# Kernel optimization log

Hardware: AMD Instinct MI355X
Metric: run time of the kernel (lower is better)

Reference implementation:

```python
import jax, jax.numpy as jnp
import numpy as np

N, E, B = 50000, 200000, 512
F0, H1, C2, EMB = 78, 10, 128, 128
SEQ, VOCAB, NF, KW = 1000, 26, 32, 8
LOUT = EMB - KW + 1  # 121


def setup_inputs() -> dict:
    key = jax.random.key(0)
    ks = jax.random.split(key, 20)
    nrm = lambda k, s: jax.random.normal(k, s, jnp.float32) * 0.05
    return dict(
        x=jax.random.normal(ks[0], (N, F0), jnp.float32),
        edge_index=jax.random.randint(ks[1], (2, E), 0, N),
        batch=(jnp.arange(N) * B) // N,  # balanced sorted node->graph ids, all segments non-empty
        target=jax.random.randint(ks[2], (B, SEQ), 0, VOCAB),
        W1=nrm(ks[3], (F0, H1 * F0)), a_src1=nrm(ks[4], (H1, F0)), a_dst1=nrm(ks[5], (H1, F0)), b1=jnp.zeros((H1 * F0,), jnp.float32),
        W2=nrm(ks[6], (H1 * F0, C2)), a_src2=nrm(ks[7], (1, C2)), a_dst2=nrm(ks[8], (1, C2)), b2=jnp.zeros((C2,), jnp.float32),
        fc_g1_w=nrm(ks[9], (C2, C2)), fc_g1_b=jnp.zeros((C2,), jnp.float32),
        emb=nrm(ks[10], (VOCAB, EMB)),
        conv_w=nrm(ks[11], (NF, SEQ, KW)), conv_b=jnp.zeros((NF,), jnp.float32),
        fc_xt_w=nrm(ks[12], (NF * LOUT, C2)), fc_xt_b=jnp.zeros((C2,), jnp.float32),
        fc1_w=nrm(ks[13], (2 * C2, 1024)), fc1_b=jnp.zeros((1024,), jnp.float32),
        fc2_w=nrm(ks[14], (1024, 256)), fc2_b=jnp.zeros((256,), jnp.float32),
        out_w=nrm(ks[15], (256, 1)), out_b=jnp.zeros((1,), jnp.float32),
    )


def gat_conv(x, src, dst, W, a_src, a_dst, b, heads):
    # PyG GATConv (eval mode): project, per-edge attn logits, segment softmax over dst, scatter-add
    n = x.shape[0]
    c = W.shape[1] // heads
    h = (x @ W).reshape(n, heads, c)                 # [N,H,C]
    al_s = (h * a_src).sum(-1)                       # [N,H]
    al_d = (h * a_dst).sum(-1)
    al = jax.nn.leaky_relu(al_s[src] + al_d[dst], 0.2)   # [E',H]
    amax = jax.ops.segment_max(al, dst, num_segments=n)
    ex = jnp.exp(al - amax[dst])
    den = jax.ops.segment_sum(ex, dst, num_segments=n)
    alpha = ex / (den[dst] + 1e-16)
    out = jax.ops.segment_sum(h[src] * alpha[:, :, None], dst, num_segments=n)  # [N,H,C]
    return out.reshape(n, heads * c) + b


def reference(x, edge_index, batch, target, W1, a_src1, a_dst1, b1, W2, a_src2, a_dst2, b2,
              fc_g1_w, fc_g1_b, emb, conv_w, conv_b, fc_xt_w, fc_xt_b,
              fc1_w, fc1_b, fc2_w, fc2_b, out_w, out_b):
    n = x.shape[0]
    loops = jnp.arange(n)
    src = jnp.concatenate([edge_index[0], loops])    # add self loops (PyG default)
    dst = jnp.concatenate([edge_index[1], loops])
    h = jax.nn.elu(gat_conv(x, src, dst, W1, a_src1, a_dst1, b1, H1))
    h = jax.nn.relu(gat_conv(h, src, dst, W2, a_src2, a_dst2, b2, 1))
    g = jax.ops.segment_max(h, batch, num_segments=B)            # global max pool per graph
    g = jax.nn.relu(g @ fc_g1_w + fc_g1_b)                       # [B,128]
    e = emb[target]                                              # [B,1000,128]
    conv = jax.lax.conv_general_dilated(e, conv_w, (1,), 'VALID',
                                        dimension_numbers=('NCH', 'OIH', 'NCH'))
    conv = jax.nn.relu(conv + conv_b[None, :, None])             # [B,32,121]
    xt = conv.reshape(B, NF * LOUT) @ fc_xt_w + fc_xt_b          # [B,128]
    xc = jnp.concatenate([g, xt], axis=1)                        # [B,256]
    xc = jax.nn.relu(xc @ fc1_w + fc1_b)
    xc = jax.nn.relu(xc @ fc2_w + fc2_b)
    return xc @ out_w + out_b                                    # [B,1]
```

## Files before the change

kernel.cpp:

```cpp
#include <hip/hip_runtime.h>
#include <hip/hip_bf16.h>

#define N_NODES 50000
#define N_EDGES 200000
#define BGRAPHS 512
#define F0c 78
#define H1c 10
#define HC1 780
#define HSTR 832
#define C2c 128
#define SEQc 1000
#define VOCABc 26
#define NFc 32
#define KWc 8
#define LOUTc 121
#define EMBc 128
#define KX 96
#define KXT 3872
#define KSTEPS2 13
#define MROWS 13312
#define KM 1024

typedef __attribute__((ext_vector_type(8))) short short8;
typedef __attribute__((ext_vector_type(4))) float f32x4;
typedef unsigned short u16;

static constexpr size_t alignup(size_t x) { return (x + 255) & ~size_t(255); }

static constexpr size_t A_HBUF = 0;
static constexpr size_t A_OUT1 = alignup(A_HBUF + size_t(N_NODES)*HSTR*2);
static constexpr size_t A_H2   = alignup(A_OUT1 + size_t(N_NODES)*HSTR*2);
static constexpr size_t A_W2T  = alignup(A_H2   + size_t(N_NODES)*C2c*4);
static constexpr size_t A_ALS1 = alignup(A_W2T  + size_t(C2c)*HSTR*2);
static constexpr size_t A_ALD1 = alignup(A_ALS1 + size_t(N_NODES)*H1c*4);
static constexpr size_t A_ALS2 = alignup(A_ALD1 + size_t(N_NODES)*H1c*4);
static constexpr size_t A_ALD2 = alignup(A_ALS2 + size_t(N_NODES)*4);
static constexpr size_t A_DEG  = alignup(A_ALD2 + size_t(N_NODES)*4);
static constexpr size_t A_OFFS = alignup(A_DEG  + size_t(N_NODES)*4);
static constexpr size_t A_CUR  = alignup(A_OFFS + size_t(N_NODES+1)*4);
static constexpr size_t A_CSRC = alignup(A_CUR  + size_t(N_NODES)*4);
static constexpr size_t A_XC   = alignup(A_CSRC + size_t(N_EDGES+N_NODES)*4);
static constexpr size_t A_Y1   = alignup(A_XC   + size_t(BGRAPHS)*256*4);
static constexpr size_t A_BOFF = alignup(A_Y1   + size_t(BGRAPHS)*1024*4);
static constexpr size_t A_BPAD = alignup(A_BOFF + size_t(BGRAPHS)*(VOCABc+1)*4);
static constexpr size_t A_WXT  = alignup(A_BPAD + size_t(HSTR)*4);
static constexpr size_t A_FXP  = alignup(A_WXT  + size_t(C2c)*KXT*2);
static constexpr size_t A_W1HP = alignup(A_FXP  + size_t(11)*BGRAPHS*C2c*4);
static constexpr size_t A_WSD  = alignup(A_W1HP + size_t(10)*80*96*2);
static constexpr size_t A_CWT  = alignup(A_WSD  + size_t(2)*H1c*F0c*4);
static constexpr size_t A_END  = alignup(A_CWT  + size_t(2)*256*KM*2);

static constexpr size_t A_HFIN = A_HBUF;
static constexpr size_t A_AMAT = alignup(A_HFIN + size_t(N_NODES)*C2c*4);
static constexpr size_t A_CVO  = alignup(A_AMAT + size_t(MROWS)*256*4);
static constexpr size_t A_M    = alignup(A_CVO  + size_t(BGRAPHS)*KXT*2);
static_assert(A_M + size_t(MROWS)*KM*2 <= size_t(N_NODES)*HSTR*2, "alias A overflow");
static constexpr size_t A_XPAD = A_OUT1;
static_assert(size_t(N_NODES)*KX*2 <= size_t(N_NODES)*HSTR*2, "alias B overflow");

__device__ __forceinline__ float bflo(unsigned u) { return __uint_as_float(u << 16); }
__device__ __forceinline__ float bfhi(unsigned u) { return __uint_as_float(u & 0xffff0000u); }
__device__ __forceinline__ u16 f2bf(float v) {
    __hip_bfloat16 b = __float2bfloat16(v);
    return *(u16*)&b;
}

#define GLOAD16(g, l) __builtin_amdgcn_global_load_lds( \
    (const __attribute__((address_space(1))) void*)(g), \
    (__attribute__((address_space(3))) void*)(l), 16, 0, 0)

__global__ void k_prep(const float* __restrict__ x, const float* __restrict__ W1,
                       const float* __restrict__ W2, const float* __restrict__ b1,
                       const float* __restrict__ fcxt_w, const float* __restrict__ conv_w,
                       const float* __restrict__ a_src1, const float* __restrict__ a_dst1,
                       __hip_bfloat16* __restrict__ xpad, __hip_bfloat16* __restrict__ w1hp,
                       __hip_bfloat16* __restrict__ w2t, float* __restrict__ bpad,
                       __hip_bfloat16* __restrict__ wxt, float* __restrict__ wsd,
                       u16* __restrict__ cwt, int* __restrict__ deg) {
    int i = blockIdx.x*256 + threadIdx.x;
    const int R0 = N_NODES;
    const int R1 = R0 + N_NODES*KX;
    const int R2 = R1 + 10*80*96;
    const int R3 = R2 + C2c*HSTR;
    const int R4 = R3 + HSTR;
    const int R5 = R4 + C2c*KXT;
    const int R6 = R5 + 2*H1c*F0c;
    const int R7 = R6 + 256*KM;
    if (i < R0) {
        deg[i] = 1;
    } else if (i < R1) {
        int t = i - R0; int n = t / KX, c = t - n*KX;
        xpad[t] = __float2bfloat16(c < F0c ? x[(size_t)n*F0c + c] : 0.f);
    } else if (i < R2) {
        int t = i - R1; int hh = t / 7680, rem = t - hh*7680;
        int j = rem / 96, k = rem - j*96;
        w1hp[t] = __float2bfloat16((j < F0c && k < F0c) ? W1[(size_t)k*HC1 + hh*F0c + j] : 0.f);
    } else if (i < R3) {
        int t = i - R2; int c = t / HSTR, p = t - c*HSTR;
        int hh = p / 80, cc = p - hh*80;
        w2t[t] = __float2bfloat16((hh < H1c && cc < F0c) ? W2[(size_t)(hh*F0c + cc)*C2c + c] : 0.f);
    } else if (i < R4) {
        int p = i - R3; int hh = p / 80, cc = p - hh*80;
        bpad[p] = (hh < H1c && cc < F0c) ? b1[hh*F0c + cc] : 0.f;
    } else if (i < R5) {
        int t = i - R4; int c = t / KXT, j = t - c*KXT;
        wxt[t] = __float2bfloat16(fcxt_w[(size_t)j*C2c + c]);
    } else if (i < R6) {
        int t = i - R5; int sd = t / (H1c*F0c), rem = t - sd*(H1c*F0c);
        int hh = rem / F0c, c = rem - hh*F0c;
        const float* a = sd ? a_dst1 : a_src1;
        float v = 0.f;
        for (int j = 0; j < F0c; j++) v += W1[(size_t)c*HC1 + hh*F0c + j] * a[hh*F0c + j];
        wsd[t] = v;
    } else if (i < R7) {
        int t = i - R6; int col = t >> 10, ii = t & (KM-1);
        int o = col >> 3, k = col & 7;
        float v = (ii < SEQc) ? conv_w[((size_t)o*SEQc + ii)*KWc + k] : 0.f;
        u16 h = f2bf(v);
        float hv = __uint_as_float((unsigned)h << 16);
        cwt[(size_t)col*KM + ii] = h;
        cwt[(size_t)256*KM + (size_t)col*KM + ii] = f2bf(v - hv);
    }
}
#define PREP_TOTAL (N_NODES + N_NODES*KX + 10*80*96 + C2c*HSTR + HSTR + C2c*KXT + 2*H1c*F0c + 256*KM)

__global__ void k_count(const int* __restrict__ ei, int* deg) {
    int i = blockIdx.x*256 + threadIdx.x;
    if (i < N_EDGES) atomicAdd(&deg[ei[N_EDGES + i]], 1);
}
__global__ void k_scan(const int* __restrict__ deg, int* __restrict__ off,
                       int* __restrict__ cur, int n) {
    __shared__ int wsum[16];
    __shared__ int s_carry;
    int tid = threadIdx.x, lane = tid & 63, wid = tid >> 6;
    if (tid == 0) s_carry = 0;
    __syncthreads();
    for (int base = 0; base < n; base += 1024) {
        int i = base + tid;
        int v0 = (i < n) ? deg[i] : 0;
        int v = v0;
        for (int d = 1; d < 64; d <<= 1) { int t = __shfl_up(v, d, 64); if (lane >= d) v += t; }
        if (lane == 63) wsum[wid] = v;
        __syncthreads();
        if (wid == 0) {
            int w = (lane < 16) ? wsum[lane] : 0;
            for (int d = 1; d < 16; d <<= 1) { int t = __shfl_up(w, d, 64); if (lane >= d) w += t; }
            if (lane < 16) wsum[lane] = w;
        }
        __syncthreads();
        int wprev = (wid > 0) ? wsum[wid-1] : 0;
        int carry = s_carry;
        if (i < n) { int o = carry + wprev + (v - v0); off[i] = o; cur[i] = o; }
        __syncthreads();
        if (tid == 0) s_carry = carry + wsum[15];
        __syncthreads();
    }
    if (tid == 0) off[n] = s_carry;
}
__global__ void k_fill(const int* __restrict__ ei, int* cur, int* __restrict__ csrc) {
    int i = blockIdx.x*256 + threadIdx.x;
    if (i < N_EDGES) {
        int s = ei[i], d = ei[N_EDGES + i];
        int p = atomicAdd(&cur[d], 1);
        csrc[p] = s;
    } else if (i < N_EDGES + N_NODES) {
        int n = i - N_EDGES;
        int p = atomicAdd(&cur[n], 1);
        csrc[p] = n;
    }
}
__global__ void k_sortcsr(const int* __restrict__ offs, int* __restrict__ csrc) {
    int n = blockIdx.x*256 + threadIdx.x;
    if (n >= N_NODES) return;
    int s = offs[n], e = offs[n+1];
    for (int i = s + 1; i < e; i++) {
        int v = csrc[i];
        int j = i - 1;
        while (j >= s && csrc[j] > v) { csrc[j+1] = csrc[j]; j--; }
        csrc[j+1] = v;
    }
}

__global__ void k_att1x(const float* __restrict__ x, const float* __restrict__ wsd,
                        float* __restrict__ als, float* __restrict__ ald) {
    int i = blockIdx.x*256 + threadIdx.x;
    if (i >= N_NODES*H1c) return;
    int n = i / H1c, hh = i - n*H1c;
    const float* xr = x + (size_t)n*F0c;
    const float* ws = wsd + hh*F0c;
    const float* wd = wsd + H1c*F0c + hh*F0c;
    float s1 = 0.f, s2 = 0.f;
    for (int c = 0; c < F0c; c++) { float v = xr[c]; s1 += v*ws[c]; s2 += v*wd[c]; }
    als[i] = s1; ald[i] = s2;
}

__global__ void k_agg1x(const unsigned* __restrict__ xpu, const float* __restrict__ als,
                        const float* __restrict__ ald, const int* __restrict__ offs,
                        const int* __restrict__ csrc, unsigned* __restrict__ xaggu) {
    constexpr int H = H1c;
    int dn = blockIdx.x, lane = threadIdx.x;
    int s = offs[dn], e = offs[dn+1], deg = e - s;
    __shared__ float wexp[64*H];
    __shared__ int   ssrc[64];
    __shared__ float ms[H], dinv_s[H];

    if (deg <= 64) {
        if (lane < deg) ssrc[lane] = csrc[s + lane];
        __syncthreads();
        for (int idx = lane; idx < deg*H; idx += 64) {
            int j = idx / H, hh = idx - j*H;
            float al = als[(size_t)ssrc[j]*H + hh] + ald[(size_t)dn*H + hh];
            wexp[idx] = (al >= 0.f) ? al : 0.2f*al;
        }
        __syncthreads();
        if (lane < H) {
            float m = -1e30f;
            for (int j = 0; j < deg; j++) m = fmaxf(m, wexp[j*H + lane]);
            float den = 0.f;
            for (int j = 0; j < deg; j++) den += __expf(wexp[j*H + lane] - m);
            ms[lane] = m; dinv_s[lane] = 1.f/(den + 1e-16f);
        }
        __syncthreads();
        for (int idx = lane; idx < deg*H; idx += 64) {
            int hh = idx % H;
            wexp[idx] = __expf(wexp[idx] - ms[hh]) * dinv_s[hh];
        }
        __syncthreads();
        if (lane < 40) {
            float accL[H], accH[H];
            #pragma unroll
            for (int hh = 0; hh < H; hh++) { accL[hh] = 0.f; accH[hh] = 0.f; }
            int j = 0;
            for (; j + 1 < deg; j += 2) {
                unsigned ua = xpu[(size_t)ssrc[j]*48 + lane];
                unsigned ub = xpu[(size_t)ssrc[j+1]*48 + lane];
                float a0 = bflo(ua), a1 = bfhi(ua), b0 = bflo(ub), b1 = bfhi(ub);
                #pragma unroll
                for (int hh = 0; hh < H; hh++) {
                    float wA = wexp[j*H + hh], wB = wexp[(j+1)*H + hh];
                    accL[hh] += wA*a0 + wB*b0;
                    accH[hh] += wA*a1 + wB*b1;
                }
            }
            if (j < deg) {
                unsigned ua = xpu[(size_t)ssrc[j]*48 + lane];
                float a0 = bflo(ua), a1 = bfhi(ua);
                #pragma unroll
                for (int hh = 0; hh < H; hh++) {
                    float wA = wexp[j*H + hh];
                    accL[hh] += wA*a0;
                    accH[hh] += wA*a1;
                }
            }
            #pragma unroll
            for (int hh = 0; hh < H; hh++) {
                unsigned p = (unsigned)f2bf(accL[hh]) | ((unsigned)f2bf(accH[hh]) << 16);
                xaggu[((size_t)dn*H + hh)*40 + lane] = p;
            }
        }
    } else {
        if (lane < H) {
            float adv = ald[(size_t)dn*H + lane];
            float m = -1e30f;
            for (int j = s; j < e; j++) {
                float al = als[(size_t)csrc[j]*H + lane] + adv;
                al = (al >= 0.f) ? al : 0.2f*al;
                m = fmaxf(m, al);
            }
            float den = 0.f;
            for (int j = s; j < e; j++) {
                float al = als[(size_t)csrc[j]*H + lane] + adv;
                al = (al >= 0.f) ? al : 0.2f*al;
                den += __expf(al - m);
            }
            ms[lane] = m; dinv_s[lane] = 1.f/(den + 1e-16f);
        }
        __syncthreads();
        if (lane < 40) {
            float accL[H], accH[H];
            #pragma unroll
            for (int hh = 0; hh < H; hh++) { accL[hh] = 0.f; accH[hh] = 0.f; }
            for (int j = s; j < e; j++) {
                int sj = csrc[j];
                unsigned ua = xpu[(size_t)sj*48 + lane];
                float a0 = bflo(ua), a1 = bfhi(ua);
                #pragma unroll
                for (int hh = 0; hh < H; hh++) {
                    float al = als[(size_t)sj*H + hh] + ald[(size_t)dn*H + hh];
                    al = (al >= 0.f) ? al : 0.2f*al;
                    float a = __expf(al - ms[hh]) * dinv_s[hh];
                    accL[hh] += a*a0;
                    accH[hh] += a*a1;
                }
            }
            #pragma unroll
            for (int hh = 0; hh < H; hh++) {
                unsigned p = (unsigned)f2bf(accL[hh]) | ((unsigned)f2bf(accH[hh]) << 16);
                xaggu[((size_t)dn*H + hh)*40 + lane] = p;
            }
        }
    }
}

__global__ void k_gemm1h(const short* __restrict__ xagg, const short* __restrict__ w1hp,
                         const float* __restrict__ bpad, u16* __restrict__ out1) {
    int wave = threadIdx.x >> 6, lane = threadIdx.x & 63;
    int m16 = lane & 15, quad = lane >> 4;
    int hh = blockIdx.y;
    int r0 = blockIdx.x*64 + wave*16;
    int rowc = min(r0 + m16, N_NODES-1);
    const short8* arow = (const short8*)(xagg + ((size_t)rowc*H1c + hh)*80);
    f32x4 acc[5];
    #pragma unroll
    for (int ct = 0; ct < 5; ct++) acc[ct] = (f32x4){0.f,0.f,0.f,0.f};
    #pragma unroll
    for (int kt = 0; kt < 3; kt++) {
        short8 af = arow[kt*4 + quad];
        #pragma unroll
        for (int ct = 0; ct < 5; ct++) {
            const short8* brow = (const short8*)(w1hp + (size_t)(hh*80 + ct*16 + m16)*96);
            short8 bf = brow[kt*4 + quad];
            acc[ct] = __builtin_amdgcn_mfma_f32_16x16x32_bf16(af, bf, acc[ct], 0, 0, 0);
        }
    }
    #pragma unroll
    for (int ct = 0; ct < 5; ct++) {
        int col = ct*16 + m16;
        float bv = bpad[hh*80 + col];
        #pragma unroll
        for (int r = 0; r < 4; r++) {
            int orow = r0 + quad*4 + r;
            if (orow < N_NODES) {
                float v = acc[ct][r] + bv;
                v = (v > 0.f) ? v : (__expf(v) - 1.f);
                out1[(size_t)orow*HSTR + hh*80 + col] = f2bf(v);
            }
        }
    }
    if (blockIdx.y == 0) {
        int rr = blockIdx.x*64 + (threadIdx.x >> 2);
        if (rr < N_NODES) {
            short8 z = (short8){0,0,0,0,0,0,0,0};
            *(short8*)&out1[(size_t)rr*HSTR + 800 + (threadIdx.x & 3)*8] = z;
        }
    }
}

__global__ void __launch_bounds__(256, 2)
k_gemm2_mfma(const short* __restrict__ A, const short* __restrict__ Bt,
             const float* __restrict__ a_src2, const float* __restrict__ a_dst2,
             float* __restrict__ Cout, float* __restrict__ als2,
             float* __restrict__ ald2) {
    __shared__ __attribute__((aligned(16))) short As[2][128*64];
    __shared__ __attribute__((aligned(16))) short Bs[2][128*64];
    int tid = threadIdx.x;
    int wave = tid >> 6, lane = tid & 63;
    int m16 = lane & 15, quad = lane >> 4;
    int blockrow = blockIdx.x * 128;

    size_t aoff[4], boff[4];
    #pragma unroll
    for (int i = 0; i < 4; i++) {
        int c = wave*256 + i*64 + lane;
        int row = c >> 3;
        int cb  = (c & 7) << 4;
        int srcb = cb ^ ((row & 7) << 4);
        int ga = blockrow + row; if (ga > N_NODES-1) ga = N_NODES-1;
        aoff[i] = (size_t)ga  * (HSTR*2) + srcb;
        boff[i] = (size_t)row * (HSTR*2) + srcb;
    }

    f32x4 acc[2][8];
    #pragma unroll
    for (int wr = 0; wr < 2; wr++)
        #pragma unroll
        for (int ct = 0; ct < 8; ct++) acc[wr][ct] = (f32x4){0.f,0.f,0.f,0.f};

    #pragma unroll
    for (int i = 0; i < 4; i++) {
        GLOAD16((const char*)A  + aoff[i], &As[0][(wave*256 + i*64)*8]);
        GLOAD16((const char*)Bt + boff[i], &Bs[0][(wave*256 + i*64)*8]);
    }
    __syncthreads();

    int cur = 0;
    int S = (m16 & 7) << 4;
    for (int s = 0; s < KSTEPS2; s++) {
        if (s + 1 < KSTEPS2) {
            size_t kb = (size_t)(s + 1) * 128;
            #pragma unroll
            for (int i = 0; i < 4; i++) {
                GLOAD16((const char*)A  + aoff[i] + kb, &As[cur^1][(wave*256 + i*64)*8]);
                GLOAD16((const char*)Bt + boff[i] + kb, &Bs[cur^1][(wave*256 + i*64)*8]);
            }
        }
        const char* asBase = (const char*)&As[cur][0];
        const char* bsBase = (const char*)&Bs[cur][0];
        #pragma unroll
        for (int kk = 0; kk < 2; kk++) {
            int kb = (kk*64 + quad*16) ^ S;
            short8 af[2];
            #pragma unroll
            for (int wr = 0; wr < 2; wr++) {
                int row = wave*32 + wr*16 + m16;
                af[wr] = *(const short8*)(asBase + row*128 + kb);
            }
            #pragma unroll
            for (int ct = 0; ct < 8; ct++) {
                int col = ct*16 + m16;
                short8 bfv = *(const short8*)(bsBase + col*128 + kb);
                acc[0][ct] = __builtin_amdgcn_mfma_f32_16x16x32_bf16(af[0], bfv, acc[0][ct], 0, 0, 0);
                acc[1][ct] = __builtin_amdgcn_mfma_f32_16x16x32_bf16(af[1], bfv, acc[1][ct], 0, 0, 0);
            }
        }
        __syncthreads();
        cur ^= 1;
    }

    float asv[8], adv[8];
    #pragma unroll
    for (int ct = 0; ct < 8; ct++) { asv[ct] = a_src2[ct*16 + m16]; adv[ct] = a_dst2[ct*16 + m16]; }
    #pragma unroll
    for (int wr = 0; wr < 2; wr++) {
        int rowbase = blockrow + wave*32 + wr*16;
        #pragma unroll
        for (int ct = 0; ct < 8; ct++) {
            int col = ct*16 + m16;
            #pragma unroll
            for (int r = 0; r < 4; r++) {
                int orow = rowbase + quad*4 + r;
                if (orow < N_NODES) Cout[(size_t)orow*C2c + col] = acc[wr][ct][r];
            }
        }
        #pragma unroll
        for (int r = 0; r < 4; r++) {
            float s1 = 0.f, s2 = 0.f;
            #pragma unroll
            for (int ct = 0; ct < 8; ct++) { s1 += acc[wr][ct][r]*asv[ct]; s2 += acc[wr][ct][r]*adv[ct]; }
            #pragma unroll
            for (int d = 1; d < 16; d <<= 1) { s1 += __shfl_xor(s1, d, 64); s2 += __shfl_xor(s2, d, 64); }
            int orow = rowbase + quad*4 + r;
            if (m16 == 0 && orow < N_NODES) { als2[orow] = s1; ald2[orow] = s2; }
        }
    }
}

__global__ void k_agg2(const float* __restrict__ h2, const float* __restrict__ als,
                       const float* __restrict__ ald, const int* __restrict__ offs,
                       const int* __restrict__ csrc, const float* __restrict__ b2,
                       float* __restrict__ out) {
    int dn = blockIdx.x, lane = threadIdx.x;
    int s = offs[dn], e = offs[dn+1], deg = e - s;
    __shared__ float wexp[128];
    __shared__ int ssrc[128];

    if (deg <= 128) {
        float adv = ald[dn];
        for (int j = lane; j < deg; j += 64) {
            int sj = csrc[s + j];
            ssrc[j] = sj;
            float al = als[sj] + adv;
            wexp[j] = (al >= 0.f) ? al : 0.2f*al;
        }
        __syncthreads();
        float m = -1e30f;
        for (int j = lane; j < deg; j += 64) m = fmaxf(m, wexp[j]);
        #pragma unroll
        for (int d = 32; d > 0; d >>= 1) m = fmaxf(m, __shfl_xor(m, d, 64));
        __syncthreads();
        float den = 0.f;
        for (int j = lane; j < deg; j += 64) {
            float ex = __expf(wexp[j] - m);
            wexp[j] = ex;
            den += ex;
        }
        #pragma unroll
        for (int d = 32; d > 0; d >>= 1) den += __shfl_xor(den, d, 64);
        float dinv = 1.f/(den + 1e-16f);
        __syncthreads();
        float2 acc = {0.f, 0.f};
        for (int j = 0; j < deg; j++) {
            float alpha = wexp[j] * dinv;
            float2 v = ((const float2*)(h2 + (size_t)ssrc[j]*C2c))[lane];
            acc.x += alpha*v.x; acc.y += alpha*v.y;
        }
        float2 o;
        o.x = fmaxf(acc.x + b2[2*lane], 0.f);
        o.y = fmaxf(acc.y + b2[2*lane+1], 0.f);
        ((float2*)(out + (size_t)dn*C2c))[lane] = o;
    } else {
        __shared__ float sm[2];
        if (lane == 0) {
            float adv = ald[dn];
            float m = -1e30f;
            for (int j = s; j < e; j++) {
                float al = als[csrc[j]] + adv;
                al = (al >= 0.f) ? al : 0.2f*al;
                m = fmaxf(m, al);
            }
            float den = 0.f;
            for (int j = s; j < e; j++) {
                float al = als[csrc[j]] + adv;
                al = (al >= 0.f) ? al : 0.2f*al;
                den += __expf(al - m);
            }
            sm[0] = m; sm[1] = 1.f/(den + 1e-16f);
        }
        __syncthreads();
        float m = sm[0], dinv = sm[1], adv = ald[dn];
        float2 acc = {0.f, 0.f};
        for (int j = s; j < e; j++) {
            int sj = csrc[j];
            float al = als[sj] + adv;
            al = (al >= 0.f) ? al : 0.2f*al;
            float alpha = __expf(al - m) * dinv;
            float2 v = ((const float2*)(h2 + (size_t)sj*C2c))[lane];
            acc.x += alpha*v.x; acc.y += alpha*v.y;
        }
        float2 o;
        o.x = fmaxf(acc.x + b2[2*lane], 0.f);
        o.y = fmaxf(acc.y + b2[2*lane+1], 0.f);
        ((float2*)(out + (size_t)dn*C2c))[lane] = o;
    }
}

__global__ void k_poolfcg(const float* __restrict__ hf, const int* __restrict__ batch,
                          const float* __restrict__ W, const float* __restrict__ bias,
                          float* __restrict__ xc) {
    int b = blockIdx.x, tid = threadIdx.x;
    __shared__ int se[2];
    __shared__ float gs[C2c];
    if (tid < 2) {
        int key = b + tid;
        int lo = 0, hi = N_NODES;
        while (lo < hi) { int mid = (lo+hi) >> 1; if (batch[mid] < key) lo = mid+1; else hi = mid; }
        se[tid] = lo;
    }
    __syncthreads();
    int s = se[0], e = se[1];
    float m = -1e30f;
    for (int n = s; n < e; n++) m = fmaxf(m, hf[(size_t)n*C2c + tid]);
    gs[tid] = m;
    __syncthreads();
    float acc = bias[tid];
    for (int k = 0; k < C2c; k++) acc += gs[k] * W[k*C2c + tid];
    xc[b*256 + tid] = fmaxf(acc, 0.f);
}

__global__ void k_buildM(const int* __restrict__ target, u16* __restrict__ Mm) {
    int b = blockIdx.x, tid = threadIdx.x;
    short8 z = (short8){0,0,0,0,0,0,0,0};
    short8* base = (short8*)(Mm + (size_t)b*VOCABc*KM);
    for (int i = tid; i < VOCABc*KM/8; i += 256) base[i] = z;
    __syncthreads();
    for (int i = tid; i < SEQc; i += 256) {
        int t = target[(size_t)b*SEQc + i];
        Mm[((size_t)b*VOCABc + t)*KM + i] = (u16)0x3F80;
    }
}

__global__ void __launch_bounds__(256, 1)
k_amat_mfma(const short* __restrict__ Mm, const short* __restrict__ cwt,
            float* __restrict__ A2) {
    __shared__ __attribute__((aligned(16))) short As[2][128*64];
    __shared__ __attribute__((aligned(16))) short Bh[2][128*64];
    __shared__ __attribute__((aligned(16))) short Bl[2][128*64];
    int tid = threadIdx.x;
    int wave = tid >> 6, lane = tid & 63;
    int m16 = lane & 15, quad = lane >> 4;
    int blockrow = blockIdx.x * 128;
    int colbase  = blockIdx.y * 128;

    size_t aoff[4], bo[4];
    #pragma unroll
    for (int i = 0; i < 4; i++) {
        int c = wave*256 + i*64 + lane;
        int row = c >> 3;
        int cb  = (c & 7) << 4;
        int srcb = cb ^ ((row & 7) << 4);
        aoff[i] = (size_t)(blockrow + row) * (KM*2) + srcb;
        bo[i]   = (size_t)(colbase  + row) * (KM*2) + srcb;
    }
    const char* hbase = (const char*)cwt;
    const char* lbase = (const char*)(cwt + (size_t)256*KM);

    f32x4 acc[2][8];
    #pragma unroll
    for (int wr = 0; wr < 2; wr++)
        #pragma unroll
        for (int ct = 0; ct < 8; ct++) acc[wr][ct] = (f32x4){0.f,0.f,0.f,0.f};

    #pragma unroll
    for (int i = 0; i < 4; i++) {
        GLOAD16((const char*)Mm + aoff[i], &As[0][(wave*256 + i*64)*8]);
        GLOAD16(hbase + bo[i],             &Bh[0][(wave*256 + i*64)*8]);
        GLOAD16(lbase + bo[i],             &Bl[0][(wave*256 + i*64)*8]);
    }
    __syncthreads();

    int cur = 0;
    int S = (m16 & 7) << 4;
    for (int s = 0; s < KM/64; s++) {
        if (s + 1 < KM/64) {
            size_t kb = (size_t)(s + 1) * 128;
            #pragma unroll
            for (int i = 0; i < 4; i++) {
                GLOAD16((const char*)Mm + aoff[i] + kb, &As[cur^1][(wave*256 + i*64)*8]);
                GLOAD16(hbase + bo[i] + kb,             &Bh[cur^1][(wave*256 + i*64)*8]);
                GLOAD16(lbase + bo[i] + kb,             &Bl[cur^1][(wave*256 + i*64)*8]);
            }
        }
        const char* asBase = (const char*)&As[cur][0];
        const char* bhBase = (const char*)&Bh[cur][0];
        const char* blBase = (const char*)&Bl[cur][0];
        #pragma unroll
        for (int kk = 0; kk < 2; kk++) {
            int kb2 = (kk*64 + quad*16) ^ S;
            short8 af[2];
            #pragma unroll
            for (int wr = 0; wr < 2; wr++) {
                int row = wave*32 + wr*16 + m16;
                af[wr] = *(const short8*)(asBase + row*128 + kb2);
            }
            #pragma unroll
            for (int ct = 0; ct < 8; ct++) {
                int col = ct*16 + m16;
                short8 bhv = *(const short8*)(bhBase + col*128 + kb2);
                short8 blv = *(const short8*)(blBase + col*128 + kb2);
                acc[0][ct] = __builtin_amdgcn_mfma_f32_16x16x32_bf16(af[0], bhv, acc[0][ct], 0, 0, 0);
                acc[1][ct] = __builtin_amdgcn_mfma_f32_16x16x32_bf16(af[1], bhv, acc[1][ct], 0, 0, 0);
                acc[0][ct] = __builtin_amdgcn_mfma_f32_16x16x32_bf16(af[0], blv, acc[0][ct], 0, 0, 0);
                acc[1][ct] = __builtin_amdgcn_mfma_f32_16x16x32_bf16(af[1], blv, acc[1][ct], 0, 0, 0);
            }
        }
        __syncthreads();
        cur ^= 1;
    }

    #pragma unroll
    for (int wr = 0; wr < 2; wr++) {
        int rowbase = blockrow + wave*32 + wr*16 + quad*4;
        #pragma unroll
        for (int ct = 0; ct < 8; ct++) {
            int col = colbase + ct*16 + m16;
            #pragma unroll
            for (int r = 0; r < 4; r++) {
                A2[(size_t)(rowbase + r)*256 + col] = acc[wr][ct][r];
            }
        }
    }
}

__global__ void __launch_bounds__(128, 4)
k_conv(const float* __restrict__ A2, const float* __restrict__ emb,
       const float* __restrict__ convb, u16* __restrict__ convout) {
    int b = blockIdx.x, og = blockIdx.y;
    int tid = threadIdx.x;
    __shared__ float embs[VOCABc*EMBc];
    __shared__ float arow[4*VOCABc*KWc];
    for (int i = tid; i < VOCABc*EMBc; i += 128) embs[i] = emb[i];
    for (int i = tid; i < 4*VOCABc*KWc; i += 128) {
        int o2 = i / (VOCABc*KWc);
        int rem = i - o2*(VOCABc*KWc);
        int t = rem >> 3, k = rem & 7;
        arow[i] = A2[((size_t)b*VOCABc + t)*256 + (og*4 + o2)*8 + k];
    }
    __syncthreads();
    if (tid < LOUTc) {
        float a0 = convb[og*4+0], a1 = convb[og*4+1], a2 = convb[og*4+2], a3 = convb[og*4+3];
        for (int t = 0; t < VOCABc; t++) {
            #pragma unroll
            for (int k = 0; k < KWc; k++) {
                float ev = embs[t*EMBc + tid + k];
                a0 += arow[0*(VOCABc*KWc) + t*KWc + k] * ev;
                a1 += arow[1*(VOCABc*KWc) + t*KWc + k] * ev;
                a2 += arow[2*(VOCABc*KWc) + t*KWc + k] * ev;
                a3 += arow[3*(VOCABc*KWc) + t*KWc + k] * ev;
            }
        }
        size_t base = (size_t)b*KXT + (og*4)*LOUTc + tid;
        convout[base            ] = f2bf(fmaxf(a0, 0.f));
        convout[base +   LOUTc  ] = f2bf(fmaxf(a1, 0.f));
        convout[base + 2*LOUTc  ] = f2bf(fmaxf(a2, 0.f));
        convout[base + 3*LOUTc  ] = f2bf(fmaxf(a3, 0.f));
    }
}
__global__ void k_fcxt_mfma(const short* __restrict__ cvo, const short* __restrict__ wxt,
                            float* __restrict__ fxp) {
    int wave = threadIdx.x >> 6, lane = threadIdx.x & 63;
    int m16 = lane & 15, quad = lane >> 4;
    int r0 = blockIdx.x*64 + wave*16;
    int kt0 = blockIdx.y*11;
    const short8* arow = (const short8*)(cvo + (size_t)(r0 + m16)*KXT);
    f32x4 acc[8];
    #pragma unroll
    for (int ct = 0; ct < 8; ct++) acc[ct] = (f32x4){0.f,0.f,0.f,0.f};
    for (int kt = kt0; kt < kt0 + 11; kt++) {
        short8 af = arow[kt*4 + quad];
        #pragma unroll
        for (int ct = 0; ct < 8; ct++) {
            const short8* brow = (const short8*)(wxt + (size_t)(ct*16 + m16)*KXT);
            short8 bf = brow[kt*4 + quad];
            acc[ct] = __builtin_amdgcn_mfma_f32_16x16x32_bf16(af, bf, acc[ct], 0, 0, 0);
        }
    }
    #pragma unroll
    for (int ct = 0; ct < 8; ct++) {
        int col = ct*16 + m16;
        #pragma unroll
        for (int r = 0; r < 4; r++) {
            int row = r0 + quad*4 + r;
            fxp[((size_t)blockIdx.y*BGRAPHS + row)*C2c + col] = acc[ct][r];
        }
    }
}

__global__ void k_fc1(const float* __restrict__ xc, const float* __restrict__ fxp,
                      const float* __restrict__ fcxt_b, const float* __restrict__ W,
                      const float* __restrict__ bias, float* __restrict__ y1) {
    int b = blockIdx.x, tid = threadIdx.x;
    __shared__ float xs[256];
    if (tid < 128) {
        xs[tid] = xc[b*256 + tid];
    } else {
        int col = tid - 128;
        float s = fcxt_b[col];
        #pragma unroll
        for (int q = 0; q < 11; q++) s += fxp[((size_t)q*BGRAPHS + b)*C2c + col];
        xs[tid] = s;
    }
    __syncthreads();
    float a0 = bias[tid], a1 = bias[tid+256], a2 = bias[tid+512], a3 = bias[tid+768];
    for (int k = 0; k < 256; k++) {
        float xk = xs[k];
        const float* wr = W + (size_t)k*1024;
        a0 += xk*wr[tid]; a1 += xk*wr[tid+256]; a2 += xk*wr[tid+512]; a3 += xk*wr[tid+768];
    }
    y1[(size_t)b*1024 + tid      ] = fmaxf(a0, 0.f);
    y1[(size_t)b*1024 + tid + 256] = fmaxf(a1, 0.f);
    y1[(size_t)b*1024 + tid + 512] = fmaxf(a2, 0.f);
    y1[(size_t)b*1024 + tid + 768] = fmaxf(a3, 0.f);
}
__global__ void k_fc2out(const float* __restrict__ y1, const float* __restrict__ W,
                         const float* __restrict__ bias, const float* __restrict__ ow,
                         const float* __restrict__ ob, float* __restrict__ out) {
    int b = blockIdx.x, tid = threadIdx.x;
    int lane = tid & 63, wid = tid >> 6;
    __shared__ float ys[1024];
    __shared__ float wsum[4];
    for (int i = tid; i < 1024; i += 256) ys[i] = y1[(size_t)b*1024 + i];
    __syncthreads();
    float acc = bias[tid];
    for (int k = 0; k < 1024; k++) acc += ys[k] * W[(size_t)k*256 + tid];
    float v = fmaxf(acc, 0.f) * ow[tid];
    #pragma unroll
    for (int d = 32; d > 0; d >>= 1) v += __shfl_xor(v, d, 64);
    if (lane == 0) wsum[wid] = v;
    __syncthreads();
    if (tid == 0) out[b] = wsum[0] + wsum[1] + wsum[2] + wsum[3] + ob[0];
}

extern "C" void kernel_launch(void* const* d_in, const int* in_sizes, int n_in,
                              void* d_out, int out_size, void* d_ws, size_t ws_size,
                              hipStream_t stream) {
    (void)in_sizes; (void)n_in; (void)out_size;
    if (ws_size < A_END) return;

    const float* x       = (const float*)d_in[0];
    const int*   ei      = (const int*)  d_in[1];
    const int*   batch   = (const int*)  d_in[2];
    const int*   target  = (const int*)  d_in[3];
    const float* W1      = (const float*)d_in[4];
    const float* a_src1  = (const float*)d_in[5];
    const float* a_dst1  = (const float*)d_in[6];
    const float* b1      = (const float*)d_in[7];
    const float* W2      = (const float*)d_in[8];
    const float* a_src2  = (const float*)d_in[9];
    const float* a_dst2  = (const float*)d_in[10];
    const float* b2      = (const float*)d_in[11];
    const float* fcg_w   = (const float*)d_in[12];
    const float* fcg_b   = (const float*)d_in[13];
    const float* emb     = (const float*)d_in[14];
    const float* conv_w  = (const float*)d_in[15];
    const float* conv_b  = (const float*)d_in[16];
    const float* fcxt_w  = (const float*)d_in[17];
    const float* fcxt_b  = (const float*)d_in[18];
    const float* fc1_w   = (const float*)d_in[19];
    const float* fc1_b   = (const float*)d_in[20];
    const float* fc2_w   = (const float*)d_in[21];
    const float* fc2_b   = (const float*)d_in[22];
    const float* out_w   = (const float*)d_in[23];
    const float* out_b   = (const float*)d_in[24];

    char* wsb = (char*)d_ws;
    u16*   xagg  = (u16*)  (wsb + A_HBUF);
    u16*   out1  = (u16*)  (wsb + A_OUT1);
    float* h2    = (float*)(wsb + A_H2);
    __hip_bfloat16* w2t = (__hip_bfloat16*)(wsb + A_W2T);
    float* als1  = (float*)(wsb + A_ALS1);
    float* ald1  = (float*)(wsb + A_ALD1);
    float* als2  = (float*)(wsb + A_ALS2);
    float* ald2  = (float*)(wsb + A_ALD2);
    int*   deg   = (int*)  (wsb + A_DEG);
    int*   offs  = (int*)  (wsb + A_OFFS);
    int*   cur   = (int*)  (wsb + A_CUR);
    int*   csrc  = (int*)  (wsb + A_CSRC);
    float* xc    = (float*)(wsb + A_XC);
    float* y1    = (float*)(wsb + A_Y1);
    float* bpad  = (float*)(wsb + A_BPAD);
    __hip_bfloat16* wxt  = (__hip_bfloat16*)(wsb + A_WXT);
    float* fxp   = (float*)(wsb + A_FXP);
    __hip_bfloat16* w1hp = (__hip_bfloat16*)(wsb + A_W1HP);
    float* wsd   = (float*)(wsb + A_WSD);
    u16*   cwt   = (u16*)  (wsb + A_CWT);
    float* hfin  = (float*)(wsb + A_HFIN);
    float* Amat2 = (float*)(wsb + A_AMAT);
    u16*   cvo   = (u16*)  (wsb + A_CVO);
    u16*   Mm    = (u16*)  (wsb + A_M);
    __hip_bfloat16* xpad = (__hip_bfloat16*)(wsb + A_XPAD);

    k_prep<<<(PREP_TOTAL+255)/256, 256, 0, stream>>>(x, W1, W2, b1, fcxt_w, conv_w,
                                                     a_src1, a_dst1,
                                                     xpad, w1hp, w2t, bpad, wxt, wsd, cwt, deg);
    k_count  <<<(N_EDGES+255)/256, 256, 0, stream>>>(ei, deg);
    k_scan   <<<1, 1024, 0, stream>>>(deg, offs, cur, N_NODES);
    k_fill   <<<(N_EDGES+N_NODES+255)/256, 256, 0, stream>>>(ei, cur, csrc);
    k_sortcsr<<<(N_NODES+255)/256, 256, 0, stream>>>(offs, csrc);

    k_att1x<<<(N_NODES*H1c+255)/256, 256, 0, stream>>>(x, wsd, als1, ald1);
    k_agg1x<<<N_NODES, 64, 0, stream>>>((const unsigned*)xpad, als1, ald1, offs, csrc,
                                        (unsigned*)xagg);
    k_gemm1h<<<dim3((N_NODES+63)/64, H1c), 256, 0, stream>>>((const short*)xagg,
                                                             (const short*)w1hp, bpad, out1);

    k_buildM<<<BGRAPHS, 256, 0, stream>>>(target, Mm);

    k_gemm2_mfma<<<(N_NODES+127)/128, 256, 0, stream>>>((const short*)out1, (const short*)w2t,
                                                        a_src2, a_dst2, h2, als2, ald2);
    k_agg2<<<N_NODES, 64, 0, stream>>>(h2, als2, ald2, offs, csrc, b2, hfin);

    k_poolfcg<<<BGRAPHS, 128, 0, stream>>>(hfin, batch, fcg_w, fcg_b, xc);

    k_amat_mfma<<<dim3(MROWS/128, 2), 256, 0, stream>>>((const short*)Mm, (const short*)cwt,
                                                        Amat2);
    k_conv  <<<dim3(BGRAPHS, 8), 128, 0, stream>>>(Amat2, emb, conv_b, cvo);
    k_fcxt_mfma<<<dim3(BGRAPHS/64, 11), 256, 0, stream>>>((const short*)cvo, (const short*)wxt, fxp);

    k_fc1<<<BGRAPHS, 256, 0, stream>>>(xc, fxp, fcxt_b, fc1_w, fc1_b, y1);
    k_fc2out<<<BGRAPHS, 256, 0, stream>>>(y1, fc2_w, fc2_b, out_w, out_b, (float*)d_out);
}
```

Measured before the change: 566.2 us.

## Fuse layer-1 per-head GEMM with layer-2 GEMM keeping activations in LDS

Merges the per-head GAT layer-1 projection (with bias and ELU) and the layer-2 projection GEMM into one kernel. Each 512-thread block computes a 64-row tile of the 832-wide layer-1 output directly into swizzled shared memory. It then multiplies that tile by the streamed W2 tiles, so the bf16 intermediate no longer goes out to global memory and back. Attention dot products are reduced across waves through shared memory. The cost is about 106KB of LDS per block, leaving one block per CU, and smaller 64-row tiles, which lowers occupancy and reuse of W2.

```diff
diff --git a/kernel.cpp b/kernel.cpp
--- a/kernel.cpp
+++ b/kernel.cpp
@@ -302,133 +302,121 @@
     }
 }
 
-__global__ void k_gemm1h(const short* __restrict__ xagg, const short* __restrict__ w1hp,
-                         const float* __restrict__ bpad, u16* __restrict__ out1) {
-    int wave = threadIdx.x >> 6, lane = threadIdx.x & 63;
-    int m16 = lane & 15, quad = lane >> 4;
-    int hh = blockIdx.y;
-    int r0 = blockIdx.x*64 + wave*16;
-    int rowc = min(r0 + m16, N_NODES-1);
-    const short8* arow = (const short8*)(xagg + ((size_t)rowc*H1c + hh)*80);
-    f32x4 acc[5];
-    #pragma unroll
-    for (int ct = 0; ct < 5; ct++) acc[ct] = (f32x4){0.f,0.f,0.f,0.f};
-    #pragma unroll
-    for (int kt = 0; kt < 3; kt++) {
-        short8 af = arow[kt*4 + quad];
-        #pragma unroll
-        for (int ct = 0; ct < 5; ct++) {
-            const short8* brow = (const short8*)(w1hp + (size_t)(hh*80 + ct*16 + m16)*96);
-            short8 bf = brow[kt*4 + quad];
-            acc[ct] = __builtin_amdgcn_mfma_f32_16x16x32_bf16(af, bf, acc[ct], 0, 0, 0);
-        }
-    }
-    #pragma unroll
-    for (int ct = 0; ct < 5; ct++) {
-        int col = ct*16 + m16;
-        float bv = bpad[hh*80 + col];
-        #pragma unroll
-        for (int r = 0; r < 4; r++) {
-            int orow = r0 + quad*4 + r;
-            if (orow < N_NODES) {
-                float v = acc[ct][r] + bv;
-                v = (v > 0.f) ? v : (__expf(v) - 1.f);
-                out1[(size_t)orow*HSTR + hh*80 + col] = f2bf(v);
-            }
-        }
-    }
-    if (blockIdx.y == 0) {
-        int rr = blockIdx.x*64 + (threadIdx.x >> 2);
-        if (rr < N_NODES) {
-            short8 z = (short8){0,0,0,0,0,0,0,0};
-            *(short8*)&out1[(size_t)rr*HSTR + 800 + (threadIdx.x & 3)*8] = z;
-        }
-    }
-}
-
-__global__ void __launch_bounds__(256, 2)
-k_gemm2_mfma(const short* __restrict__ A, const short* __restrict__ Bt,
-             const float* __restrict__ a_src2, const float* __restrict__ a_dst2,
-             float* __restrict__ Cout, float* __restrict__ als2,
-             float* __restrict__ ald2) {
-    __shared__ __attribute__((aligned(16))) short As[2][128*64];
+__global__ void __launch_bounds__(512, 1)
+k_fuse12(const short* __restrict__ xagg, const short* __restrict__ w1hp,
+         const float* __restrict__ bpad, const short* __restrict__ Bt,
+         const float* __restrict__ a_src2, const float* __restrict__ a_dst2,
+         float* __restrict__ Cout, float* __restrict__ als2, float* __restrict__ ald2) {
+    __shared__ __attribute__((aligned(16))) short As[64*832];
     __shared__ __attribute__((aligned(16))) short Bs[2][128*64];
+    __shared__ float sred[64][4], sredd[64][4];
     int tid = threadIdx.x;
     int wave = tid >> 6, lane = tid & 63;
     int m16 = lane & 15, quad = lane >> 4;
-    int blockrow = blockIdx.x * 128;
-
-    size_t aoff[4], boff[4];
-    #pragma unroll
-    for (int i = 0; i < 4; i++) {
-        int c = wave*256 + i*64 + lane;
-        int row = c >> 3;
-        int cb  = (c & 7) << 4;
-        int srcb = cb ^ ((row & 7) << 4);
-        int ga = blockrow + row; if (ga > N_NODES-1) ga = N_NODES-1;
-        aoff[i] = (size_t)ga  * (HSTR*2) + srcb;
-        boff[i] = (size_t)row * (HSTR*2) + srcb;
-    }
-
-    f32x4 acc[2][8];
+    int blockrow = blockIdx.x * 64;
+
+    size_t boff2[2];
+    #pragma unroll
+    for (int j = 0; j < 2; j++) {
+        int c = wave*64 + j*512 + lane;
+        int row = c >> 3, cb = (c & 7) << 4;
+        boff2[j] = (size_t)row*(HSTR*2) + (cb ^ ((row & 7) << 4));
+        GLOAD16((const char*)Bt + boff2[j], &Bs[0][(wave*64 + j*512)*8]);
+    }
+
+    {
+        int wg = (wave >> 1) * 16;
+        int h0 = (wave & 1) * 5;
+        int rowc = min(blockrow + wg + m16, N_NODES-1);
+        for (int hh = h0; hh < h0 + 5; hh++) {
+            const short8* arow = (const short8*)(xagg + ((size_t)rowc*H1c + hh)*80);
+            f32x4 acc1[5];
+            #pragma unroll
+            for (int ct = 0; ct < 5; ct++) acc1[ct] = (f32x4){0.f,0.f,0.f,0.f};
+            #pragma unroll
+            for (int kt = 0; kt < 3; kt++) {
+                short8 af = arow[kt*4 + quad];
+                #pragma unroll
+                for (int ct = 0; ct < 5; ct++) {
+                    const short8* brow = (const short8*)(w1hp + (size_t)(hh*80 + ct*16 + m16)*96);
+                    acc1[ct] = __builtin_amdgcn_mfma_f32_16x16x32_bf16(af, brow[kt*4 + quad],
+                                                                      acc1[ct], 0, 0, 0);
+                }
+            }
+            #pragma unroll
+            for (int ct = 0; ct < 5; ct++) {
+                int col = hh*80 + ct*16 + m16;
+                float bv = bpad[col];
+                #pragma unroll
+                for (int r = 0; r < 4; r++) {
+                    int rl = wg + quad*4 + r;
+                    float v = acc1[ct][r] + bv;
+                    v = (v > 0.f) ? v : (__expf(v) - 1.f);
+                    *(u16*)((char*)As + rl*1664 + ((col*2) ^ ((rl & 7) << 4))) = f2bf(v);
+                }
+            }
+        }
+    }
+    for (int e = tid; e < 64*32; e += 512) {
+        int rl = e >> 5, cc = 800 + (e & 31);
+        *(u16*)((char*)As + rl*1664 + ((cc*2) ^ ((rl & 7) << 4))) = 0;
+    }
+    __syncthreads();
+
+    int rg = (wave >> 2) * 32;
+    int ch = (wave & 3) * 32;
+    f32x4 acc[2][2];
     #pragma unroll
     for (int wr = 0; wr < 2; wr++)
         #pragma unroll
-        for (int ct = 0; ct < 8; ct++) acc[wr][ct] = (f32x4){0.f,0.f,0.f,0.f};
-
-    #pragma unroll
-    for (int i = 0; i < 4; i++) {
-        GLOAD16((const char*)A  + aoff[i], &As[0][(wave*256 + i*64)*8]);
-        GLOAD16((const char*)Bt + boff[i], &Bs[0][(wave*256 + i*64)*8]);
-    }
-    __syncthreads();
-
+        for (int ct = 0; ct < 2; ct++) acc[wr][ct] = (f32x4){0.f,0.f,0.f,0.f};
+
+    int S = (m16 & 7) << 4;
     int cur = 0;
-    int S = (m16 & 7) << 4;
     for (int s = 0; s < KSTEPS2; s++) {
         if (s + 1 < KSTEPS2) {
             size_t kb = (size_t)(s + 1) * 128;
             #pragma unroll
-            for (int i = 0; i < 4; i++) {
-                GLOAD16((const char*)A  + aoff[i] + kb, &As[cur^1][(wave*256 + i*64)*8]);
-                GLOAD16((const char*)Bt + boff[i] + kb, &Bs[cur^1][(wave*256 + i*64)*8]);
-            }
-        }
-        const char* asBase = (const char*)&As[cur][0];
-        const char* bsBase = (const char*)&Bs[cur][0];
+            for (int j = 0; j < 2; j++)
+                GLOAD16((const char*)Bt + boff2[j] + kb, &Bs[cur^1][(wave*64 + j*512)*8]);
+        }
+        const char* asB = (const char*)As + (size_t)s*128;
+        const char* bsB = (const char*)&Bs[cur][0];
         #pragma unroll
         for (int kk = 0; kk < 2; kk++) {
-            int kb = (kk*64 + quad*16) ^ S;
-            short8 af[2];
-            #pragma unroll
-            for (int wr = 0; wr < 2; wr++) {
-                int row = wave*32 + wr*16 + m16;
-                af[wr] = *(const short8*)(asBase + row*128 + kb);
-            }
-            #pragma unroll
-            for (int ct = 0; ct < 8; ct++) {
-                int col = ct*16 + m16;
-                short8 bfv = *(const short8*)(bsBase + col*128 + kb);
-                acc[0][ct] = __builtin_amdgcn_mfma_f32_16x16x32_bf16(af[0], bfv, acc[0][ct], 0, 0, 0);
-                acc[1][ct] = __builtin_amdgcn_mfma_f32_16x16x32_bf16(af[1], bfv, acc[1][ct], 0, 0, 0);
-            }
+            int kb2 = (kk*64 + quad*16) ^ S;
+            short8 af[2], bfv[2];
+            #pragma unroll
+            for (int wr = 0; wr < 2; wr++)
+                af[wr] = *(const short8*)(asB + (rg + wr*16 + m16)*1664 + kb2);
+            #pragma unroll
+            for (int ct = 0; ct < 2; ct++)
+                bfv[ct] = *(const short8*)(bsB + (ch + ct*16 + m16)*128 + kb2);
+            #pragma unroll
+            for (int wr = 0; wr < 2; wr++)
+                #pragma unroll
+                for (int ct = 0; ct < 2; ct++)
+                    acc[wr][ct] = __builtin_amdgcn_mfma_f32_16x16x32_bf16(af[wr], bfv[ct],
+                                                                         acc[wr][ct], 0, 0, 0);
         }
         __syncthreads();
         cur ^= 1;
     }
 
-    float asv[8], adv[8];
-    #pragma unroll
-    for (int ct = 0; ct < 8; ct++) { asv[ct] = a_src2[ct*16 + m16]; adv[ct] = a_dst2[ct*16 + m16]; }
+    float asv[2], adv[2];
+    #pragma unroll
+    for (int ct = 0; ct < 2; ct++) {
+        asv[ct] = a_src2[ch + ct*16 + m16];
+        adv[ct] = a_dst2[ch + ct*16 + m16];
+    }
     #pragma unroll
     for (int wr = 0; wr < 2; wr++) {
-        int rowbase = blockrow + wave*32 + wr*16;
-        #pragma unroll
-        for (int ct = 0; ct < 8; ct++) {
-            int col = ct*16 + m16;
+        #pragma unroll
+        for (int ct = 0; ct < 2; ct++) {
+            int col = ch + ct*16 + m16;
             #pragma unroll
             for (int r = 0; r < 4; r++) {
-                int orow = rowbase + quad*4 + r;
+                int orow = blockrow + rg + wr*16 + quad*4 + r;
                 if (orow < N_NODES) Cout[(size_t)orow*C2c + col] = acc[wr][ct][r];
             }
         }
@@ -436,11 +424,22 @@
         for (int r = 0; r < 4; r++) {
             float s1 = 0.f, s2 = 0.f;
             #pragma unroll
-            for (int ct = 0; ct < 8; ct++) { s1 += acc[wr][ct][r]*asv[ct]; s2 += acc[wr][ct][r]*adv[ct]; }
+            for (int ct = 0; ct < 2; ct++) { s1 += acc[wr][ct][r]*asv[ct]; s2 += acc[wr][ct][r]*adv[ct]; }
             #pragma unroll
             for (int d = 1; d < 16; d <<= 1) { s1 += __shfl_xor(s1, d, 64); s2 += __shfl_xor(s2, d, 64); }
-            int orow = rowbase + quad*4 + r;
-            if (m16 == 0 && orow < N_NODES) { als2[orow] = s1; ald2[orow] = s2; }
+            if (m16 == 0) {
+                int rl = rg + wr*16 + quad*4 + r;
+                sred[rl][wave & 3] = s1;
+                sredd[rl][wave & 3] = s2;
+            }
+        }
+    }
+    __syncthreads();
+    if (tid < 64) {
+        int orow = blockrow + tid;
+        if (orow < N_NODES) {
+            als2[orow] = sred[tid][0] + sred[tid][1] + sred[tid][2] + sred[tid][3];
+            ald2[orow] = sredd[tid][0] + sredd[tid][1] + sredd[tid][2] + sredd[tid][3];
         }
     }
 }
@@ -794,7 +793,6 @@
 
     char* wsb = (char*)d_ws;
     u16*   xagg  = (u16*)  (wsb + A_HBUF);
-    u16*   out1  = (u16*)  (wsb + A_OUT1);
     float* h2    = (float*)(wsb + A_H2);
     __hip_bfloat16* w2t = (__hip_bfloat16*)(wsb + A_W2T);
     float* als1  = (float*)(wsb + A_ALS1);
@@ -830,13 +828,13 @@
     k_att1x<<<(N_NODES*H1c+255)/256, 256, 0, stream>>>(x, wsd, als1, ald1);
     k_agg1x<<<N_NODES, 64, 0, stream>>>((const unsigned*)xpad, als1, ald1, offs, csrc,
                                         (unsigned*)xagg);
-    k_gemm1h<<<dim3((N_NODES+63)/64, H1c), 256, 0, stream>>>((const short*)xagg,
-                                                             (const short*)w1hp, bpad, out1);
+
+    k_fuse12<<<(N_NODES+63)/64, 512, 0, stream>>>((const short*)xagg, (const short*)w1hp,
+                                                  bpad, (const short*)w2t,
+                                                  a_src2, a_dst2, h2, als2, ald2);
 
     k_buildM<<<BGRAPHS, 256, 0, stream>>>(target, Mm);
 
-    k_gemm2_mfma<<<(N_NODES+127)/128, 256, 0, stream>>>((const short*)out1, (const short*)w2t,
-                                                        a_src2, a_dst2, h2, als2, ald2);
     k_agg2<<<N_NODES, 64, 0, stream>>>(h2, als2, ald2, offs, csrc, b2, hfin);
 
     k_poolfcg<<<BGRAPHS, 128, 0, stream>>>(hfin, batch, fcg_w, fcg_b, xc);
```

Result: no change. 574.2 us (+1.4%).
